# Optimization experiments

Hardware: AMD Instinct MI355X
Metric: run time of the kernel (lower is better)

Reference implementation:

```python
import jax, jax.numpy as jnp
import numpy as np

B = 2
D_MODEL = 256
D_FFN = 1024
N_LEVELS = 4
N_HEADS = 8
N_POINTS = 4
D_HEAD = D_MODEL // N_HEADS
SHAPES = np.array([[128, 128], [64, 64], [32, 32], [16, 16]], dtype=np.int32)  # (H, W) per level
LEN = int(SHAPES.prod(axis=1).sum())  # 21760
EPS = 1e-5


def _layer_norm(x, g, b):
    m = jnp.mean(x, axis=-1, keepdims=True)
    v = jnp.mean(jnp.square(x - m), axis=-1, keepdims=True)
    return (x - m) * jax.lax.rsqrt(v + EPS) * g + b


def _bilinear_gather(v_l, loc, H, W):
    # v_l: [B, H*W, NH, DH]; loc: [B, L, NH, NP, 2] in normalized [0,1] coords (x, y)
    # grid_sample(align_corners=False, padding_mode=zeros) semantics: pixel = loc * size - 0.5
    x = loc[..., 0] * W - 0.5
    y = loc[..., 1] * H - 0.5
    x0 = jnp.floor(x)
    y0 = jnp.floor(y)
    dx = x - x0
    dy = y - y0
    x0i = x0.astype(jnp.int32)
    y0i = y0.astype(jnp.int32)
    b_ix = jnp.arange(v_l.shape[0])[:, None, None, None]
    h_ix = jnp.arange(v_l.shape[2])[None, None, :, None]

    def corner(xi, yi, w):
        valid = (xi >= 0) & (xi < W) & (yi >= 0) & (yi < H)
        idx = jnp.clip(yi, 0, H - 1) * W + jnp.clip(xi, 0, W - 1)
        v = v_l[b_ix, idx, h_ix]  # [B, L, NH, NP, DH]
        return v * (w * valid.astype(v.dtype))[..., None]

    return (corner(x0i, y0i, (1 - dx) * (1 - dy))
            + corner(x0i + 1, y0i, dx * (1 - dy))
            + corner(x0i, y0i + 1, (1 - dx) * dy)
            + corner(x0i + 1, y0i + 1, dx * dy))


def _forward(src, pos, reference_points,
             w_off, b_off, w_attn, b_attn, w_val, b_val, w_out, b_out,
             ln1_g, ln1_b, w1, b1, w2, b2, ln2_g, ln2_b,
             spatial_shapes, level_start_index, padding_mask):
    shapes = np.asarray(spatial_shapes)        # static per-level (H, W)
    starts = np.asarray(level_start_index)     # static level offsets
    Bsz, L, _ = src.shape

    # ---- MSDeformAttn ----
    q = src + pos                              # with_pos_embed
    value = src @ w_val + b_val
    value = jnp.where(padding_mask[..., None], 0.0, value)
    value = value.reshape(Bsz, L, N_HEADS, D_HEAD)

    off = (q @ w_off + b_off).reshape(Bsz, L, N_HEADS, N_LEVELS, N_POINTS, 2)
    attn = (q @ w_attn + b_attn).reshape(Bsz, L, N_HEADS, N_LEVELS * N_POINTS)
    attn = jax.nn.softmax(attn, axis=-1).reshape(Bsz, L, N_HEADS, N_LEVELS, N_POINTS)

    wh = jnp.asarray(shapes[:, ::-1].copy(), dtype=src.dtype)  # [NL, 2] = (W, H)
    loc = reference_points[:, :, None, :, None, :] + off / wh[None, None, None, :, None, :]

    out = jnp.zeros((Bsz, L, N_HEADS, D_HEAD), src.dtype)
    for l in range(N_LEVELS):
        H, W = int(shapes[l, 0]), int(shapes[l, 1])
        s = int(starts[l])
        v_l = value[:, s:s + H * W]                          # [B, H*W, NH, DH]
        sampled = _bilinear_gather(v_l, loc[:, :, :, l], H, W)  # [B, L, NH, NP, DH]
        out = out + (sampled * attn[:, :, :, l][..., None]).sum(axis=3)
    attn_out = out.reshape(Bsz, L, D_MODEL) @ w_out + b_out

    # ---- residual + LN + FFN + residual + LN (dropout = identity in eval) ----
    x = _layer_norm(src + attn_out, ln1_g, ln1_b)
    ffn = jax.nn.relu(x @ w1 + b1) @ w2 + b2
    return _layer_norm(x + ffn, ln2_g, ln2_b)


def setup_inputs() -> dict:
    key = jax.random.key(0)
    ks = jax.random.split(key, 16)
    s = 0.02
    n_off = N_HEADS * N_LEVELS * N_POINTS
    level_start = np.concatenate([[0], SHAPES.prod(axis=1).cumsum()[:-1]]).astype(np.int32)
    return {
        "src": jax.random.normal(ks[0], (B, LEN, D_MODEL), jnp.float32),
        "pos": jax.random.normal(ks[1], (B, LEN, D_MODEL), jnp.float32),
        "reference_points": jax.random.uniform(ks[2], (B, LEN, N_LEVELS, 2), jnp.float32),
        "spatial_shapes": jnp.asarray(SHAPES),
        "level_start_index": jnp.asarray(level_start),
        "padding_mask": jnp.zeros((B, LEN), jnp.bool_),
        "w_off": jax.random.normal(ks[3], (D_MODEL, n_off * 2), jnp.float32) * s,
        "b_off": jax.random.normal(ks[4], (n_off * 2,), jnp.float32) * 0.5,
        "w_attn": jax.random.normal(ks[5], (D_MODEL, n_off), jnp.float32) * s,
        "b_attn": jnp.zeros((n_off,), jnp.float32),
        "w_val": jax.random.normal(ks[6], (D_MODEL, D_MODEL), jnp.float32) * s,
        "b_val": jnp.zeros((D_MODEL,), jnp.float32),
        "w_out": jax.random.normal(ks[7], (D_MODEL, D_MODEL), jnp.float32) * s,
        "b_out": jnp.zeros((D_MODEL,), jnp.float32),
        "ln1_g": jnp.ones((D_MODEL,), jnp.float32),
        "ln1_b": jnp.zeros((D_MODEL,), jnp.float32),
        "w1": jax.random.normal(ks[8], (D_MODEL, D_FFN), jnp.float32) * s,
        "b1": jnp.zeros((D_FFN,), jnp.float32),
        "w2": jax.random.normal(ks[9], (D_FFN, D_MODEL), jnp.float32) * s,
        "b2": jnp.zeros((D_MODEL,), jnp.float32),
        "ln2_g": jnp.ones((D_MODEL,), jnp.float32),
        "ln2_b": jnp.zeros((D_MODEL,), jnp.float32),
    }


def reference(src, pos, reference_points, spatial_shapes, level_start_index, padding_mask,
              w_off, b_off, w_attn, b_attn, w_val, b_val, w_out, b_out,
              ln1_g, ln1_b, w1, b1, w2, b2, ln2_g, ln2_b):
    return _forward(src, pos, reference_points,
                    w_off, b_off, w_attn, b_attn, w_val, b_val, w_out, b_out,
                    ln1_g, ln1_b, w1, b1, w2, b2, ln2_g, ln2_b,
                    spatial_shapes, level_start_index, padding_mask)
```

## Files before the change

kernel.cpp:

```cpp
#include <hip/hip_runtime.h>
#include <hip/hip_bf16.h>

#define BSZ      2
#define LTOK     21760
#define NTOK     (BSZ * LTOK)
#define DMODEL   256
#define DFFN     1024

typedef __attribute__((ext_vector_type(8))) short short8;
typedef __attribute__((ext_vector_type(4))) float f32x4;

__device__ __forceinline__ unsigned short f2bf(float x) {
    __hip_bfloat16 h = __float2bfloat16(x);
    return *reinterpret_cast<unsigned short*>(&h);
}
__device__ __forceinline__ float bf2f(unsigned short u) {
    union { unsigned int i; float f; } c; c.i = ((unsigned int)u) << 16; return c.f;
}
__device__ __forceinline__ float bflo(unsigned int u) {
    union { unsigned int i; float f; } c; c.i = u << 16; return c.f;
}
__device__ __forceinline__ float bfhi(unsigned int u) {
    union { unsigned int i; float f; } c; c.i = u & 0xffff0000u; return c.f;
}

#define TM 128
#define TN 256
#define TBK 32
#define EBS 264

__device__ __forceinline__ void gemm_core(
    const unsigned short* __restrict__ A,
    const unsigned short* __restrict__ Bt,
    unsigned short* sA, unsigned short* sB,
    int bm, int bn, int N, int K,
    int tid, int lane, int wm, int wn,
    f32x4 acc[4][8])
{
    const int sr = tid >> 6;
    const int fr = lane & 15;
    const int fk = (lane >> 4) * 8;

    for (int k0 = 0; k0 < K; k0 += TBK) {
        #pragma unroll
        for (int rr = 0; rr < 2; ++rr) {
            const int s = sr + rr * 4;
            const size_t grow = (size_t)(bm + s * 16 + fr);
            *(uint4*)&sA[s * 512 + lane * 8] = *(const uint4*)(A + grow * K + k0 + fk);
        }
        #pragma unroll
        for (int rr = 0; rr < 4; ++rr) {
            const int s = sr + rr * 4;
            int gn = bn + s * 16 + fr;
            gn = min(gn, N - 1);
            *(uint4*)&sB[s * 512 + lane * 8] = *(const uint4*)(Bt + (size_t)gn * K + k0 + fk);
        }
        __syncthreads();

        short8 af[4], bfr[8];
        #pragma unroll
        for (int i = 0; i < 4; ++i)
            af[i] = *(const short8*)&sA[(wm * 4 + i) * 512 + lane * 8];
        #pragma unroll
        for (int j = 0; j < 8; ++j)
            bfr[j] = *(const short8*)&sB[(wn * 8 + j) * 512 + lane * 8];
        #pragma unroll
        for (int i = 0; i < 4; ++i)
            #pragma unroll
            for (int j = 0; j < 8; ++j)
                acc[i][j] = __builtin_amdgcn_mfma_f32_16x16x32_bf16(
                    af[i], bfr[j], acc[i][j], 0, 0, 0);
        __syncthreads();
    }
}

__global__ __launch_bounds__(256, 2) void gemm_mfma(
    const unsigned short* __restrict__ A,
    const unsigned short* __restrict__ Bt, const float* __restrict__ bias,
    unsigned short* __restrict__ Cb,
    int M, int N, int K, int relu)
{
    __shared__ __align__(16) unsigned short smem[TM * TBK + TN * TBK];
    const int tid  = threadIdx.x;
    const int lane = tid & 63;
    const int wave = tid >> 6;
    const int wm = wave >> 1, wn = wave & 1;
    const int bm = blockIdx.y * TM;
    const int bn = blockIdx.x * TN;

    f32x4 acc[4][8];
    #pragma unroll
    for (int i = 0; i < 4; ++i)
        #pragma unroll
        for (int j = 0; j < 8; ++j)
            acc[i][j] = (f32x4){0.f, 0.f, 0.f, 0.f};

    gemm_core(A, Bt, smem, smem + TM * TBK, bm, bn, N, K, tid, lane, wm, wn, acc);

    const int r0 = (lane >> 4) * 4;
    const int c0 = lane & 15;
    unsigned short* eb = smem;
    #pragma unroll
    for (int i = 0; i < 4; ++i) {
        if (i) __syncthreads();
        #pragma unroll
        for (int j = 0; j < 8; ++j) {
            const int col = bn + wn * 128 + j * 16 + c0;
            const float bj = (col < N) ? bias[col] : 0.f;
            #pragma unroll
            for (int r = 0; r < 4; ++r) {
                float v = acc[i][j][r] + bj;
                if (relu) v = fmaxf(v, 0.f);
                eb[(wm * 16 + r0 + r) * EBS + wn * 128 + j * 16 + c0] = f2bf(v);
            }
        }
        __syncthreads();
        #pragma unroll
        for (int qq = 0; qq < 4; ++qq) {
            const int q  = tid + qq * 256;
            const int rl = q >> 5;
            const int ch = q & 31;
            const int grow = bm + (rl >> 4) * 64 + i * 16 + (rl & 15);
            const int colb = bn + ch * 8;
            if (colb < N)
                *(uint4*)&Cb[(size_t)grow * N + colb] =
                    *(const uint4*)&eb[rl * EBS + ch * 8];
        }
    }
}

__global__ __launch_bounds__(256, 2) void gemm_proj(
    const unsigned short* __restrict__ A0, const unsigned short* __restrict__ B0,
    const float* __restrict__ bias0, unsigned short* __restrict__ C0,
    const unsigned char* __restrict__ mask,
    const unsigned short* __restrict__ A1, const unsigned short* __restrict__ B1,
    const float* __restrict__ bias1, unsigned short* __restrict__ C1)
{
    __shared__ __align__(16) unsigned short smem[TM * TBK + TN * TBK];
    const int tid  = threadIdx.x;
    const int lane = tid & 63;
    const int wave = tid >> 6;
    const int wm = wave >> 1, wn = wave & 1;
    const int bm = blockIdx.y * TM;
    const int bx = blockIdx.x;

    const int isv = (bx == 0);
    const unsigned short* A    = isv ? A0 : A1;
    const unsigned short* Bt   = isv ? B0 : B1;
    const float*          bias = isv ? bias0 : bias1;
    const int N  = isv ? 256 : 384;
    const int bn = isv ? 0 : (bx - 1) * 256;
    const int K  = 256;

    f32x4 acc[4][8];
    #pragma unroll
    for (int i = 0; i < 4; ++i)
        #pragma unroll
        for (int j = 0; j < 8; ++j)
            acc[i][j] = (f32x4){0.f, 0.f, 0.f, 0.f};

    gemm_core(A, Bt, smem, smem + TM * TBK, bm, bn, N, K, tid, lane, wm, wn, acc);

    const int r0 = (lane >> 4) * 4;
    const int c0 = lane & 15;
    unsigned short* eb = smem;
    #pragma unroll
    for (int i = 0; i < 4; ++i) {
        if (i) __syncthreads();
        #pragma unroll
        for (int j = 0; j < 8; ++j) {
            const int col = bn + wn * 128 + j * 16 + c0;
            const float bj = (col < N) ? bias[col] : 0.f;
            #pragma unroll
            for (int r = 0; r < 4; ++r) {
                const int row = bm + wm * 64 + i * 16 + r0 + r;
                float v = acc[i][j][r] + bj;
                if (isv && mask[row]) v = 0.f;
                eb[(wm * 16 + r0 + r) * EBS + wn * 128 + j * 16 + c0] = f2bf(v);
            }
        }
        __syncthreads();
        #pragma unroll
        for (int qq = 0; qq < 4; ++qq) {
            const int q  = tid + qq * 256;
            const int rl = q >> 5;
            const int ch = q & 31;
            const int grow = bm + (rl >> 4) * 64 + i * 16 + (rl & 15);
            const int colb = bn + ch * 8;
            if (colb < N) {
                const uint4 val = *(const uint4*)&eb[rl * EBS + ch * 8];
                if (isv) {
                    const int bb   = grow >= LTOK;
                    const int srow = grow - bb * LTOK;
                    const int hcol = ch >> 2;
                    const int d    = (ch & 3) * 8;
                    *(uint4*)&C0[((size_t)(bb * 8 + hcol) * LTOK + srow) * 32 + d] = val;
                } else {
                    *(uint4*)&C1[(size_t)grow * 384 + colb] = val;
                }
            }
        }
    }
}

__global__ __launch_bounds__(256, 2) void gemm_ln(
    const unsigned short* __restrict__ A,
    const unsigned short* __restrict__ Bt, const float* __restrict__ bias,
    const unsigned short* __restrict__ resid,
    const float* __restrict__ g, const float* __restrict__ be,
    float* __restrict__ outF, unsigned short* __restrict__ outB, int K)
{
    __shared__ __align__(16) unsigned short smem[TM * TBK + TN * TBK];
    const int tid  = threadIdx.x;
    const int lane = tid & 63;
    const int wave = tid >> 6;
    const int wm = wave >> 1, wn = wave & 1;
    const int bm = blockIdx.y * TM;

    f32x4 acc[4][8];
    #pragma unroll
    for (int i = 0; i < 4; ++i)
        #pragma unroll
        for (int j = 0; j < 8; ++j)
            acc[i][j] = (f32x4){0.f, 0.f, 0.f, 0.f};

    gemm_core(A, Bt, smem, smem + TM * TBK, bm, 0, 256, K, tid, lane, wm, wn, acc);

    const int r0 = (lane >> 4) * 4;
    const int c0 = lane & 15;
    unsigned short* eb = smem;

    #pragma unroll
    for (int i = 0; i < 4; ++i) {
        if (i) __syncthreads();
        #pragma unroll
        for (int j = 0; j < 8; ++j) {
            const int col = wn * 128 + j * 16 + c0;
            const float bj = bias[col];
            #pragma unroll
            for (int r = 0; r < 4; ++r)
                eb[(wm * 16 + r0 + r) * EBS + col] = f2bf(acc[i][j][r] + bj);
        }
        __syncthreads();

        const int row = tid >> 3;
        const int l   = tid & 7;
        const int grow = bm + (row >> 4) * 64 + i * 16 + (row & 15);
        const unsigned short* rr = resid + (size_t)grow * 256 + l * 32;

        float s = 0.f, sq = 0.f;
        #pragma unroll
        for (int k = 0; k < 4; ++k) {
            const uint4 e = *(const uint4*)&eb[row * EBS + l * 32 + k * 8];
            const uint4 rv = *(const uint4*)(rr + k * 8);
            const unsigned int eu[4] = {e.x, e.y, e.z, e.w};
            const unsigned int ru[4] = {rv.x, rv.y, rv.z, rv.w};
            #pragma unroll
            for (int q = 0; q < 4; ++q) {
                const float v0 = bflo(eu[q]) + bflo(ru[q]);
                const float v1 = bfhi(eu[q]) + bfhi(ru[q]);
                s += v0 + v1;
                sq += v0 * v0 + v1 * v1;
            }
        }
        #pragma unroll
        for (int m = 4; m; m >>= 1) {
            s  += __shfl_xor(s, m, 8);
            sq += __shfl_xor(sq, m, 8);
        }
        const float mean = s * (1.f / 256.f);
        const float var  = sq * (1.f / 256.f) - mean * mean;
        const float rs   = rsqrtf(var + 1e-5f);

        #pragma unroll
        for (int k = 0; k < 4; ++k) {
            const int col = l * 32 + k * 8;
            const uint4 e = *(const uint4*)&eb[row * EBS + col];
            const uint4 rv = *(const uint4*)(rr + k * 8);
            const unsigned int eu[4] = {e.x, e.y, e.z, e.w};
            const unsigned int ru[4] = {rv.x, rv.y, rv.z, rv.w};
            float o[8];
            #pragma unroll
            for (int q = 0; q < 4; ++q) {
                const float g0 = g[col + q * 2],     b0 = be[col + q * 2];
                const float g1 = g[col + q * 2 + 1], b1 = be[col + q * 2 + 1];
                o[q * 2]     = (bflo(eu[q]) + bflo(ru[q]) - mean) * rs * g0 + b0;
                o[q * 2 + 1] = (bfhi(eu[q]) + bfhi(ru[q]) - mean) * rs * g1 + b1;
            }
            if (outB) {
                uint4 pk;
                pk.x = (unsigned)f2bf(o[0]) | ((unsigned)f2bf(o[1]) << 16);
                pk.y = (unsigned)f2bf(o[2]) | ((unsigned)f2bf(o[3]) << 16);
                pk.z = (unsigned)f2bf(o[4]) | ((unsigned)f2bf(o[5]) << 16);
                pk.w = (unsigned)f2bf(o[6]) | ((unsigned)f2bf(o[7]) << 16);
                *(uint4*)(outB + (size_t)grow * 256 + col) = pk;
            } else {
                float4 f0 = make_float4(o[0], o[1], o[2], o[3]);
                float4 f1 = make_float4(o[4], o[5], o[6], o[7]);
                *(float4*)(outF + (size_t)grow * 256 + col) = f0;
                *(float4*)(outF + (size_t)grow * 256 + col + 4) = f1;
            }
        }
        __syncthreads();
    }
}

__global__ __launch_bounds__(256) void prepass(
    const float* __restrict__ src, const float* __restrict__ pos,
    unsigned short* __restrict__ sb, unsigned short* __restrict__ qs)
{
    const size_t i = ((size_t)blockIdx.x * 256 + threadIdx.x) * 4;
    const float4 s = *(const float4*)(src + i);
    const float4 p = *(const float4*)(pos + i);
    ushort4 us, uq;
    us.x = f2bf(s.x); us.y = f2bf(s.y); us.z = f2bf(s.z); us.w = f2bf(s.w);
    uq.x = f2bf(s.x + p.x); uq.y = f2bf(s.y + p.y);
    uq.z = f2bf(s.z + p.z); uq.w = f2bf(s.w + p.w);
    *(ushort4*)(sb + i) = us;
    *(ushort4*)(qs + i) = uq;
}

__global__ void transpose_all(
    const float* __restrict__ w_val, const float* __restrict__ w_off,
    const float* __restrict__ w_att, const float* __restrict__ w_out,
    const float* __restrict__ w1,    const float* __restrict__ w2,
    const float* __restrict__ b_off, const float* __restrict__ b_att,
    unsigned short* __restrict__ wvalT, unsigned short* __restrict__ woaT,
    unsigned short* __restrict__ woutT, unsigned short* __restrict__ w1T,
    unsigned short* __restrict__ w2T,   float* __restrict__ bcat)
{
    const int blk = blockIdx.x;
    const int tx = threadIdx.x, ty = threadIdx.y;
    if (blk == 736) {
        const int t = ty * 32 + tx;
        bcat[t] = (t < 256) ? b_off[t] : b_att[t - 256];
        if (t + 256 < 384) bcat[t + 256] = b_att[t];
        return;
    }
    const float* W; unsigned short* Wt; int K, N, base;
    if      (blk < 64)  { W = w_val; Wt = wvalT;           K = 256;  N = 256;  base = 0;   }
    else if (blk < 128) { W = w_off; Wt = woaT;            K = 256;  N = 256;  base = 64;  }
    else if (blk < 160) { W = w_att; Wt = woaT + 256*256;  K = 256;  N = 128;  base = 128; }
    else if (blk < 224) { W = w_out; Wt = woutT;           K = 256;  N = 256;  base = 160; }
    else if (blk < 480) { W = w1;    Wt = w1T;             K = 256;  N = 1024; base = 224; }
    else                { W = w2;    Wt = w2T;             K = 1024; N = 256;  base = 480; }
    const int local = blk - base;
    const int kb = local % (K / 32);
    const int nb = local / (K / 32);
    const int k0 = kb * 32, n0 = nb * 32;

    __shared__ float t[32][33];
    #pragma unroll
    for (int i = 0; i < 32; i += 8)
        t[ty + i][tx] = W[(size_t)(k0 + ty + i) * N + n0 + tx];
    __syncthreads();
    #pragma unroll
    for (int i = 0; i < 32; i += 8)
        Wt[(size_t)(n0 + ty + i) * K + k0 + tx] = f2bf(t[tx][ty + i]);
}

__global__ __launch_bounds__(256) void sample_kernel(
    const unsigned short* __restrict__ vT, const unsigned short* __restrict__ qp,
    const float* __restrict__ ref,
    const int* __restrict__ sshapes, const int* __restrict__ lstart,
    unsigned short* __restrict__ samp)
{
    __shared__ __align__(16) int   s_o[256][4];
    __shared__ __align__(16) float s_w[256][4];

    const int blk   = blockIdx.x;
    const int plane = blk & 15;
    const int chunk = blk >> 4;
    const int b = plane >> 3;
    const int h = plane & 7;
    const int s0 = chunk * 16;
    const int t = threadIdx.x;

    {
        const int tl = t >> 4;
        const int p  = t & 15;
        const int l  = p >> 2;
        const int pp = p & 3;
        const int H = sshapes[2 * l], W = sshapes[2 * l + 1];
        const float Wf = (float)W, Hf = (float)H;
        const size_t tok = (size_t)(b * LTOK + s0 + tl);

        const float ox = bf2f(qp[tok * 384 + h * 32 + l * 8 + pp * 2 + 0]);
        const float oy = bf2f(qp[tok * 384 + h * 32 + l * 8 + pp * 2 + 1]);
        const float rx = ref[tok * 8 + l * 2 + 0];
        const float ry = ref[tok * 8 + l * 2 + 1];

        const float x = (rx + ox / Wf) * Wf - 0.5f;
        const float y = (ry + oy / Hf) * Hf - 0.5f;
        const float x0 = floorf(x), y0 = floorf(y);
        const float dx = x - x0, dy = y - y0;
        const int x0i = (int)x0, y0i = (int)y0;
        const int s = lstart[l];

        const float a = bf2f(qp[tok * 384 + 256 + h * 16 + p]);
        float mx = a;
        #pragma unroll
        for (int m = 8; m; m >>= 1) mx = fmaxf(mx, __shfl_xor(mx, m, 16));
        const float e = __expf(a - mx);
        float ssum = e;
        #pragma unroll
        for (int m = 8; m; m >>= 1) ssum += __shfl_xor(ssum, m, 16);
        const float prob = e / ssum;

        const float cw[4] = {(1.f - dx) * (1.f - dy), dx * (1.f - dy),
                             (1.f - dx) * dy,         dx * dy};
        const int cx[4] = {x0i, x0i + 1, x0i,     x0i + 1};
        const int cy[4] = {y0i, y0i,     y0i + 1, y0i + 1};
        int4   o4;
        float4 w4;
        #pragma unroll
        for (int c = 0; c < 4; ++c) {
            const bool valid = (cx[c] >= 0) & (cx[c] < W) & (cy[c] >= 0) & (cy[c] < H);
            const int xi = min(max(cx[c], 0), W - 1);
            const int yi = min(max(cy[c], 0), H - 1);
            ((int*)&o4)[c]   = (s + yi * W + xi) * 64;
            ((float*)&w4)[c] = valid ? cw[c] * prob : 0.f;
        }
        const int r = p * 16 + tl;
        *(int4*)&s_o[r][0]   = o4;
        *(float4*)&s_w[r][0] = w4;
    }
    __syncthreads();

    const int tl = t >> 4;
    const int dp = t & 15;
    const char* vp = (const char*)(vT + (size_t)plane * LTOK * 32) + dp * 4;
    float acc0 = 0.f, acc1 = 0.f;
    #pragma unroll
    for (int p = 0; p < 16; ++p) {
        const int r = p * 16 + tl;
        const int4   o4 = *(const int4*)&s_o[r][0];
        const float4 w4 = *(const float4*)&s_w[r][0];
        const unsigned int u0 = *(const unsigned int*)(vp + o4.x);
        const unsigned int u1 = *(const unsigned int*)(vp + o4.y);
        const unsigned int u2 = *(const unsigned int*)(vp + o4.z);
        const unsigned int u3 = *(const unsigned int*)(vp + o4.w);
        acc0 = fmaf(w4.x, bflo(u0), acc0); acc1 = fmaf(w4.x, bfhi(u0), acc1);
        acc0 = fmaf(w4.y, bflo(u1), acc0); acc1 = fmaf(w4.y, bfhi(u1), acc1);
        acc0 = fmaf(w4.z, bflo(u2), acc0); acc1 = fmaf(w4.z, bfhi(u2), acc1);
        acc0 = fmaf(w4.w, bflo(u3), acc0); acc1 = fmaf(w4.w, bfhi(u3), acc1);
    }
    const unsigned int o = (unsigned)f2bf(acc0) | ((unsigned)f2bf(acc1) << 16);
    *(unsigned int*)(samp + (size_t)(b * LTOK + s0 + tl) * 256 + h * 32 + dp * 2) = o;
}

extern "C" void kernel_launch(void* const* d_in, const int* in_sizes, int n_in,
                              void* d_out, int out_size, void* d_ws, size_t ws_size,
                              hipStream_t stream)
{
    const float* src   = (const float*)d_in[0];
    const float* pos   = (const float*)d_in[1];
    const float* ref   = (const float*)d_in[2];
    const int*   sshap = (const int*)d_in[3];
    const int*   lstrt = (const int*)d_in[4];
    const unsigned char* mask = (const unsigned char*)d_in[5];
    const float* w_off = (const float*)d_in[6];
    const float* b_off = (const float*)d_in[7];
    const float* w_att = (const float*)d_in[8];
    const float* b_att = (const float*)d_in[9];
    const float* w_val = (const float*)d_in[10];
    const float* b_val = (const float*)d_in[11];
    const float* w_out = (const float*)d_in[12];
    const float* b_out = (const float*)d_in[13];
    const float* ln1g  = (const float*)d_in[14];
    const float* ln1b  = (const float*)d_in[15];
    const float* w1    = (const float*)d_in[16];
    const float* b1    = (const float*)d_in[17];
    const float* w2    = (const float*)d_in[18];
    const float* b2    = (const float*)d_in[19];
    const float* ln2g  = (const float*)d_in[20];
    const float* ln2b  = (const float*)d_in[21];
    float* out = (float*)d_out;

    const size_t HSZ = (size_t)NTOK * 256 * 2;
    char* w = (char*)d_ws;
    unsigned short* qs     = (unsigned short*)w;
    unsigned short* samp16 = (unsigned short*)w;
    unsigned short* qpb    = (unsigned short*)(w + HSZ);
    unsigned short* vT     = (unsigned short*)(w + HSZ * 5 / 2);
    unsigned short* hidb   = (unsigned short*)w;
    unsigned short* sb     = (unsigned short*)(w + HSZ * 9 / 2);
    unsigned short* xb     = (unsigned short*)(w + HSZ * 11 / 2);
    char* wreg = w + HSZ * 13 / 2;
    unsigned short* wvalT  = (unsigned short*)wreg;
    unsigned short* woaT   = wvalT + 256 * 256;
    unsigned short* woutT  = woaT + 384 * 256;
    unsigned short* w1T    = woutT + 256 * 256;
    unsigned short* w2T    = w1T + 1024 * 256;
    float*          bcat   = (float*)(w2T + 256 * 1024);

    const dim3 blk(256);

    prepass<<<dim3(NTOK / 4), blk, 0, stream>>>(src, pos, sb, qs);

    transpose_all<<<dim3(737), dim3(32, 8), 0, stream>>>(
        w_val, w_off, w_att, w_out, w1, w2, b_off, b_att,
        wvalT, woaT, woutT, w1T, w2T, bcat);

    gemm_proj<<<dim3(3, NTOK / TM), blk, 0, stream>>>(
        sb, wvalT, b_val, vT, mask, qs, woaT, bcat, qpb);

    sample_kernel<<<dim3(16 * (LTOK / 16)), blk, 0, stream>>>(
        vT, qpb, ref, sshap, lstrt, samp16);

    gemm_ln<<<dim3(1, NTOK / TM), blk, 0, stream>>>(
        samp16, woutT, b_out, sb, ln1g, ln1b, nullptr, xb, 256);

    gemm_mfma<<<dim3(4, NTOK / TM), blk, 0, stream>>>(
        xb, w1T, b1, hidb, NTOK, DFFN, 256, 1);

    gemm_ln<<<dim3(1, NTOK / TM), blk, 0, stream>>>(
        hidb, w2T, b2, xb, ln2g, ln2b, out, nullptr, DFFN);
}
```

Before: 480.4 us.

## Double-buffer GEMM LDS tiles with direct global-to-LDS async loads

The shared GEMM core now loads tiles with global_load_lds, which writes straight into LDS without going through registers, and keeps two LDS buffers so the next K-tile is fetched while MFMAs run on the current one. Row pointers are computed once outside the K loop. The aim is to hide global memory latency and cut the register traffic in the GEMM kernels. In exchange LDS use per block doubles, which may lower occupancy, and correctness relies on the ordering of the async LDS writes and waits around the barriers.

```diff
diff --git a/kernel.cpp b/kernel.cpp
--- a/kernel.cpp
+++ b/kernel.cpp
@@ -24,15 +24,55 @@
     union { unsigned int i; float f; } c; c.i = u & 0xffff0000u; return c.f;
 }
 
+__device__ __forceinline__ void gload_lds16(const void* g, void* l) {
+    __builtin_amdgcn_global_load_lds(
+        (const __attribute__((address_space(1))) unsigned int*)g,
+        (__attribute__((address_space(3))) unsigned int*)l, 16, 0, 0);
+}
+
 #define TM 128
 #define TN 256
 #define TBK 32
+#define BUFSZ (TM * TBK + TN * TBK)
 #define EBS 264
+
+__device__ __forceinline__ void stage_tile(
+    const unsigned short* aR0, const unsigned short* aR1,
+    const unsigned short* bR0, const unsigned short* bR1,
+    const unsigned short* bR2, const unsigned short* bR3,
+    int k0, unsigned short* sA, unsigned short* sB, int sr)
+{
+    gload_lds16(aR0 + k0, &sA[(sr + 0)  * 512]);
+    gload_lds16(aR1 + k0, &sA[(sr + 4)  * 512]);
+    gload_lds16(bR0 + k0, &sB[(sr + 0)  * 512]);
+    gload_lds16(bR1 + k0, &sB[(sr + 4)  * 512]);
+    gload_lds16(bR2 + k0, &sB[(sr + 8)  * 512]);
+    gload_lds16(bR3 + k0, &sB[(sr + 12) * 512]);
+}
+
+__device__ __forceinline__ void compute_tile(
+    const unsigned short* sA, const unsigned short* sB,
+    int lane, int wm, int wn, f32x4 acc[4][8])
+{
+    short8 af[4], bfr[8];
+    #pragma unroll
+    for (int i = 0; i < 4; ++i)
+        af[i] = *(const short8*)&sA[(wm * 4 + i) * 512 + lane * 8];
+    #pragma unroll
+    for (int j = 0; j < 8; ++j)
+        bfr[j] = *(const short8*)&sB[(wn * 8 + j) * 512 + lane * 8];
+    #pragma unroll
+    for (int i = 0; i < 4; ++i)
+        #pragma unroll
+        for (int j = 0; j < 8; ++j)
+            acc[i][j] = __builtin_amdgcn_mfma_f32_16x16x32_bf16(
+                af[i], bfr[j], acc[i][j], 0, 0, 0);
+}
 
 __device__ __forceinline__ void gemm_core(
     const unsigned short* __restrict__ A,
     const unsigned short* __restrict__ Bt,
-    unsigned short* sA, unsigned short* sB,
+    unsigned short* smem,
     int bm, int bn, int N, int K,
     int tid, int lane, int wm, int wn,
     f32x4 acc[4][8])
@@ -41,35 +81,29 @@
     const int fr = lane & 15;
     const int fk = (lane >> 4) * 8;
 
-    for (int k0 = 0; k0 < K; k0 += TBK) {
-        #pragma unroll
-        for (int rr = 0; rr < 2; ++rr) {
-            const int s = sr + rr * 4;
-            const size_t grow = (size_t)(bm + s * 16 + fr);
-            *(uint4*)&sA[s * 512 + lane * 8] = *(const uint4*)(A + grow * K + k0 + fk);
-        }
-        #pragma unroll
-        for (int rr = 0; rr < 4; ++rr) {
-            const int s = sr + rr * 4;
-            int gn = bn + s * 16 + fr;
-            gn = min(gn, N - 1);
-            *(uint4*)&sB[s * 512 + lane * 8] = *(const uint4*)(Bt + (size_t)gn * K + k0 + fk);
-        }
+    const unsigned short* aR0 = A + (size_t)(bm + (sr + 0) * 16 + fr) * K + fk;
+    const unsigned short* aR1 = A + (size_t)(bm + (sr + 4) * 16 + fr) * K + fk;
+    const unsigned short* bR0 = Bt + (size_t)min(bn + (sr + 0)  * 16 + fr, N - 1) * K + fk;
+    const unsigned short* bR1 = Bt + (size_t)min(bn + (sr + 4)  * 16 + fr, N - 1) * K + fk;
+    const unsigned short* bR2 = Bt + (size_t)min(bn + (sr + 8)  * 16 + fr, N - 1) * K + fk;
+    const unsigned short* bR3 = Bt + (size_t)min(bn + (sr + 12) * 16 + fr, N - 1) * K + fk;
+
+    unsigned short* sA0 = smem;
+    unsigned short* sB0 = smem + TM * TBK;
+    unsigned short* sA1 = smem + BUFSZ;
+    unsigned short* sB1 = smem + BUFSZ + TM * TBK;
+
+    stage_tile(aR0, aR1, bR0, bR1, bR2, bR3, 0, sA0, sB0, sr);
+    __syncthreads();
+
+    for (int k0 = 0; k0 < K; k0 += 2 * TBK) {
+        if (k0 + TBK < K)
+            stage_tile(aR0, aR1, bR0, bR1, bR2, bR3, k0 + TBK, sA1, sB1, sr);
+        compute_tile(sA0, sB0, lane, wm, wn, acc);
         __syncthreads();
-
-        short8 af[4], bfr[8];
-        #pragma unroll
-        for (int i = 0; i < 4; ++i)
-            af[i] = *(const short8*)&sA[(wm * 4 + i) * 512 + lane * 8];
-        #pragma unroll
-        for (int j = 0; j < 8; ++j)
-            bfr[j] = *(const short8*)&sB[(wn * 8 + j) * 512 + lane * 8];
-        #pragma unroll
-        for (int i = 0; i < 4; ++i)
-            #pragma unroll
-            for (int j = 0; j < 8; ++j)
-                acc[i][j] = __builtin_amdgcn_mfma_f32_16x16x32_bf16(
-                    af[i], bfr[j], acc[i][j], 0, 0, 0);
+        if (k0 + 2 * TBK < K)
+            stage_tile(aR0, aR1, bR0, bR1, bR2, bR3, k0 + 2 * TBK, sA0, sB0, sr);
+        compute_tile(sA1, sB1, lane, wm, wn, acc);
         __syncthreads();
     }
 }
@@ -80,7 +114,7 @@
     unsigned short* __restrict__ Cb,
     int M, int N, int K, int relu)
 {
-    __shared__ __align__(16) unsigned short smem[TM * TBK + TN * TBK];
+    __shared__ __align__(16) unsigned short smem[2 * BUFSZ];
     const int tid  = threadIdx.x;
     const int lane = tid & 63;
     const int wave = tid >> 6;
@@ -95,7 +129,7 @@
         for (int j = 0; j < 8; ++j)
             acc[i][j] = (f32x4){0.f, 0.f, 0.f, 0.f};
 
-    gemm_core(A, Bt, smem, smem + TM * TBK, bm, bn, N, K, tid, lane, wm, wn, acc);
+    gemm_core(A, Bt, smem, bm, bn, N, K, tid, lane, wm, wn, acc);
 
     const int r0 = (lane >> 4) * 4;
     const int c0 = lane & 15;
@@ -136,7 +170,7 @@
     const unsigned short* __restrict__ A1, const unsigned short* __restrict__ B1,
     const float* __restrict__ bias1, unsigned short* __restrict__ C1)
 {
-    __shared__ __align__(16) unsigned short smem[TM * TBK + TN * TBK];
+    __shared__ __align__(16) unsigned short smem[2 * BUFSZ];
     const int tid  = threadIdx.x;
     const int lane = tid & 63;
     const int wave = tid >> 6;
@@ -159,7 +193,7 @@
         for (int j = 0; j < 8; ++j)
             acc[i][j] = (f32x4){0.f, 0.f, 0.f, 0.f};
 
-    gemm_core(A, Bt, smem, smem + TM * TBK, bm, bn, N, K, tid, lane, wm, wn, acc);
+    gemm_core(A, Bt, smem, bm, bn, N, K, tid, lane, wm, wn, acc);
 
     const int r0 = (lane >> 4) * 4;
     const int c0 = lane & 15;
@@ -210,7 +244,7 @@
     const float* __restrict__ g, const float* __restrict__ be,
     float* __restrict__ outF, unsigned short* __restrict__ outB, int K)
 {
-    __shared__ __align__(16) unsigned short smem[TM * TBK + TN * TBK];
+    __shared__ __align__(16) unsigned short smem[2 * BUFSZ];
     const int tid  = threadIdx.x;
     const int lane = tid & 63;
     const int wave = tid >> 6;
@@ -224,7 +258,7 @@
         for (int j = 0; j < 8; ++j)
             acc[i][j] = (f32x4){0.f, 0.f, 0.f, 0.f};
 
-    gemm_core(A, Bt, smem, smem + TM * TBK, bm, 0, 256, K, tid, lane, wm, wn, acc);
+    gemm_core(A, Bt, smem, bm, 0, 256, K, tid, lane, wm, wn, acc);
 
     const int r0 = (lane >> 4) * 4;
     const int c0 = lane & 15;
```

Result: no change. 482.6 us (+0.5%).

## Use 512-thread GEMM blocks with direct global-to-LDS loads

Applied to the files above, without the earlier changes.

Doubles the GEMM workgroup size to 8 waves, so each wave owns a 64x64 output sub-tile instead of 64x128. This halves accumulator registers and allows more concurrent waves. Tile loads now use global_load_lds to write straight into shared memory without passing through registers. The epilogue and LayerNorm reductions are remapped to the new thread count. Smaller per-wave tiles mean more LDS fragment reads per MFMA, and there is still no double buffering.

```diff
diff --git a/kernel.cpp b/kernel.cpp
--- a/kernel.cpp
+++ b/kernel.cpp
@@ -24,6 +24,12 @@
     union { unsigned int i; float f; } c; c.i = u & 0xffff0000u; return c.f;
 }
 
+__device__ __forceinline__ void gload_lds16(const void* g, void* l) {
+    __builtin_amdgcn_global_load_lds(
+        (const __attribute__((address_space(1))) unsigned int*)g,
+        (__attribute__((address_space(3))) unsigned int*)l, 16, 0, 0);
+}
+
 #define TM 128
 #define TN 256
 #define TBK 32
@@ -32,49 +38,46 @@
 __device__ __forceinline__ void gemm_core(
     const unsigned short* __restrict__ A,
     const unsigned short* __restrict__ Bt,
-    unsigned short* sA, unsigned short* sB,
+    unsigned short* smem,
     int bm, int bn, int N, int K,
     int tid, int lane, int wm, int wn,
-    f32x4 acc[4][8])
+    f32x4 acc[4][4])
 {
     const int sr = tid >> 6;
     const int fr = lane & 15;
     const int fk = (lane >> 4) * 8;
 
+    const unsigned short* aR  = A  + (size_t)(bm + sr * 16 + fr) * K + fk;
+    const unsigned short* bR0 = Bt + (size_t)min(bn + sr * 16 + fr,       N - 1) * K + fk;
+    const unsigned short* bR1 = Bt + (size_t)min(bn + (sr + 8) * 16 + fr, N - 1) * K + fk;
+
+    unsigned short* sA = smem;
+    unsigned short* sB = smem + TM * TBK;
+
     for (int k0 = 0; k0 < K; k0 += TBK) {
-        #pragma unroll
-        for (int rr = 0; rr < 2; ++rr) {
-            const int s = sr + rr * 4;
-            const size_t grow = (size_t)(bm + s * 16 + fr);
-            *(uint4*)&sA[s * 512 + lane * 8] = *(const uint4*)(A + grow * K + k0 + fk);
-        }
-        #pragma unroll
-        for (int rr = 0; rr < 4; ++rr) {
-            const int s = sr + rr * 4;
-            int gn = bn + s * 16 + fr;
-            gn = min(gn, N - 1);
-            *(uint4*)&sB[s * 512 + lane * 8] = *(const uint4*)(Bt + (size_t)gn * K + k0 + fk);
-        }
+        gload_lds16(aR  + k0, &sA[sr * 512]);
+        gload_lds16(bR0 + k0, &sB[sr * 512]);
+        gload_lds16(bR1 + k0, &sB[(sr + 8) * 512]);
         __syncthreads();
 
-        short8 af[4], bfr[8];
+        short8 af[4], bfr[4];
         #pragma unroll
         for (int i = 0; i < 4; ++i)
             af[i] = *(const short8*)&sA[(wm * 4 + i) * 512 + lane * 8];
         #pragma unroll
-        for (int j = 0; j < 8; ++j)
-            bfr[j] = *(const short8*)&sB[(wn * 8 + j) * 512 + lane * 8];
+        for (int j = 0; j < 4; ++j)
+            bfr[j] = *(const short8*)&sB[(wn * 4 + j) * 512 + lane * 8];
         #pragma unroll
         for (int i = 0; i < 4; ++i)
             #pragma unroll
-            for (int j = 0; j < 8; ++j)
+            for (int j = 0; j < 4; ++j)
                 acc[i][j] = __builtin_amdgcn_mfma_f32_16x16x32_bf16(
                     af[i], bfr[j], acc[i][j], 0, 0, 0);
         __syncthreads();
     }
 }
 
-__global__ __launch_bounds__(256, 2) void gemm_mfma(
+__global__ __launch_bounds__(512, 4) void gemm_mfma(
     const unsigned short* __restrict__ A,
     const unsigned short* __restrict__ Bt, const float* __restrict__ bias,
     unsigned short* __restrict__ Cb,
@@ -84,18 +87,18 @@
     const int tid  = threadIdx.x;
     const int lane = tid & 63;
     const int wave = tid >> 6;
-    const int wm = wave >> 1, wn = wave & 1;
+    const int wm = wave >> 2, wn = wave & 3;
     const int bm = blockIdx.y * TM;
     const int bn = blockIdx.x * TN;
 
-    f32x4 acc[4][8];
+    f32x4 acc[4][4];
     #pragma unroll
     for (int i = 0; i < 4; ++i)
         #pragma unroll
-        for (int j = 0; j < 8; ++j)
+        for (int j = 0; j < 4; ++j)
             acc[i][j] = (f32x4){0.f, 0.f, 0.f, 0.f};
 
-    gemm_core(A, Bt, smem, smem + TM * TBK, bm, bn, N, K, tid, lane, wm, wn, acc);
+    gemm_core(A, Bt, smem, bm, bn, N, K, tid, lane, wm, wn, acc);
 
     const int r0 = (lane >> 4) * 4;
     const int c0 = lane & 15;
@@ -104,20 +107,20 @@
     for (int i = 0; i < 4; ++i) {
         if (i) __syncthreads();
         #pragma unroll
-        for (int j = 0; j < 8; ++j) {
-            const int col = bn + wn * 128 + j * 16 + c0;
+        for (int j = 0; j < 4; ++j) {
+            const int col = bn + wn * 64 + j * 16 + c0;
             const float bj = (col < N) ? bias[col] : 0.f;
             #pragma unroll
             for (int r = 0; r < 4; ++r) {
                 float v = acc[i][j][r] + bj;
                 if (relu) v = fmaxf(v, 0.f);
-                eb[(wm * 16 + r0 + r) * EBS + wn * 128 + j * 16 + c0] = f2bf(v);
+                eb[(wm * 16 + r0 + r) * EBS + wn * 64 + j * 16 + c0] = f2bf(v);
             }
         }
         __syncthreads();
         #pragma unroll
-        for (int qq = 0; qq < 4; ++qq) {
-            const int q  = tid + qq * 256;
+        for (int qq = 0; qq < 2; ++qq) {
+            const int q  = tid + qq * 512;
             const int rl = q >> 5;
             const int ch = q & 31;
             const int grow = bm + (rl >> 4) * 64 + i * 16 + (rl & 15);
@@ -129,7 +132,7 @@
     }
 }
 
-__global__ __launch_bounds__(256, 2) void gemm_proj(
+__global__ __launch_bounds__(512, 4) void gemm_proj(
     const unsigned short* __restrict__ A0, const unsigned short* __restrict__ B0,
     const float* __restrict__ bias0, unsigned short* __restrict__ C0,
     const unsigned char* __restrict__ mask,
@@ -140,7 +143,7 @@
     const int tid  = threadIdx.x;
     const int lane = tid & 63;
     const int wave = tid >> 6;
-    const int wm = wave >> 1, wn = wave & 1;
+    const int wm = wave >> 2, wn = wave & 3;
     const int bm = blockIdx.y * TM;
     const int bx = blockIdx.x;
 
@@ -152,14 +155,14 @@
     const int bn = isv ? 0 : (bx - 1) * 256;
     const int K  = 256;
 
-    f32x4 acc[4][8];
+    f32x4 acc[4][4];
     #pragma unroll
     for (int i = 0; i < 4; ++i)
         #pragma unroll
-        for (int j = 0; j < 8; ++j)
+        for (int j = 0; j < 4; ++j)
             acc[i][j] = (f32x4){0.f, 0.f, 0.f, 0.f};
 
-    gemm_core(A, Bt, smem, smem + TM * TBK, bm, bn, N, K, tid, lane, wm, wn, acc);
+    gemm_core(A, Bt, smem, bm, bn, N, K, tid, lane, wm, wn, acc);
 
     const int r0 = (lane >> 4) * 4;
     const int c0 = lane & 15;
@@ -168,21 +171,21 @@
     for (int i = 0; i < 4; ++i) {
         if (i) __syncthreads();
         #pragma unroll
-        for (int j = 0; j < 8; ++j) {
-            const int col = bn + wn * 128 + j * 16 + c0;
+        for (int j = 0; j < 4; ++j) {
+            const int col = bn + wn * 64 + j * 16 + c0;
             const float bj = (col < N) ? bias[col] : 0.f;
             #pragma unroll
             for (int r = 0; r < 4; ++r) {
                 const int row = bm + wm * 64 + i * 16 + r0 + r;
                 float v = acc[i][j][r] + bj;
                 if (isv && mask[row]) v = 0.f;
-                eb[(wm * 16 + r0 + r) * EBS + wn * 128 + j * 16 + c0] = f2bf(v);
+                eb[(wm * 16 + r0 + r) * EBS + wn * 64 + j * 16 + c0] = f2bf(v);
             }
         }
         __syncthreads();
         #pragma unroll
-        for (int qq = 0; qq < 4; ++qq) {
-            const int q  = tid + qq * 256;
+        for (int qq = 0; qq < 2; ++qq) {
+            const int q  = tid + qq * 512;
             const int rl = q >> 5;
             const int ch = q & 31;
             const int grow = bm + (rl >> 4) * 64 + i * 16 + (rl & 15);
@@ -203,7 +206,7 @@
     }
 }
 
-__global__ __launch_bounds__(256, 2) void gemm_ln(
+__global__ __launch_bounds__(512, 4) void gemm_ln(
     const unsigned short* __restrict__ A,
     const unsigned short* __restrict__ Bt, const float* __restrict__ bias,
     const unsigned short* __restrict__ resid,
@@ -214,17 +217,17 @@
     const int tid  = threadIdx.x;
     const int lane = tid & 63;
     const int wave = tid >> 6;
-    const int wm = wave >> 1, wn = wave & 1;
+    const int wm = wave >> 2, wn = wave & 3;
     const int bm = blockIdx.y * TM;
 
-    f32x4 acc[4][8];
+    f32x4 acc[4][4];
     #pragma unroll
     for (int i = 0; i < 4; ++i)
         #pragma unroll
-        for (int j = 0; j < 8; ++j)
+        for (int j = 0; j < 4; ++j)
             acc[i][j] = (f32x4){0.f, 0.f, 0.f, 0.f};
 
-    gemm_core(A, Bt, smem, smem + TM * TBK, bm, 0, 256, K, tid, lane, wm, wn, acc);
+    gemm_core(A, Bt, smem, bm, 0, 256, K, tid, lane, wm, wn, acc);
 
     const int r0 = (lane >> 4) * 4;
     const int c0 = lane & 15;
@@ -234,8 +237,8 @@
     for (int i = 0; i < 4; ++i) {
         if (i) __syncthreads();
         #pragma unroll
-        for (int j = 0; j < 8; ++j) {
-            const int col = wn * 128 + j * 16 + c0;
+        for (int j = 0; j < 4; ++j) {
+            const int col = wn * 64 + j * 16 + c0;
             const float bj = bias[col];
             #pragma unroll
             for (int r = 0; r < 4; ++r)
@@ -243,15 +246,15 @@
         }
         __syncthreads();
 
-        const int row = tid >> 3;
-        const int l   = tid & 7;
+        const int row = tid >> 4;
+        const int l   = tid & 15;
         const int grow = bm + (row >> 4) * 64 + i * 16 + (row & 15);
-        const unsigned short* rr = resid + (size_t)grow * 256 + l * 32;
+        const unsigned short* rr = resid + (size_t)grow * 256 + l * 16;
 
         float s = 0.f, sq = 0.f;
         #pragma unroll
-        for (int k = 0; k < 4; ++k) {
-            const uint4 e = *(const uint4*)&eb[row * EBS + l * 32 + k * 8];
+        for (int k = 0; k < 2; ++k) {
+            const uint4 e = *(const uint4*)&eb[row * EBS + l * 16 + k * 8];
             const uint4 rv = *(const uint4*)(rr + k * 8);
             const unsigned int eu[4] = {e.x, e.y, e.z, e.w};
             const unsigned int ru[4] = {rv.x, rv.y, rv.z, rv.w};
@@ -264,17 +267,17 @@
             }
         }
         #pragma unroll
-        for (int m = 4; m; m >>= 1) {
-            s  += __shfl_xor(s, m, 8);
-            sq += __shfl_xor(sq, m, 8);
+        for (int m = 8; m; m >>= 1) {
+            s  += __shfl_xor(s, m, 16);
+            sq += __shfl_xor(sq, m, 16);
         }
         const float mean = s * (1.f / 256.f);
         const float var  = sq * (1.f / 256.f) - mean * mean;
         const float rs   = rsqrtf(var + 1e-5f);
 
         #pragma unroll
-        for (int k = 0; k < 4; ++k) {
-            const int col = l * 32 + k * 8;
+        for (int k = 0; k < 2; ++k) {
+            const int col = l * 16 + k * 8;
             const uint4 e = *(const uint4*)&eb[row * EBS + col];
             const uint4 rv = *(const uint4*)(rr + k * 8);
             const unsigned int eu[4] = {e.x, e.y, e.z, e.w};
@@ -495,6 +498,7 @@
     float*          bcat   = (float*)(w2T + 256 * 1024);
 
     const dim3 blk(256);
+    const dim3 blk512(512);
 
     prepass<<<dim3(NTOK / 4), blk, 0, stream>>>(src, pos, sb, qs);
 
@@ -502,18 +506,18 @@
         w_val, w_off, w_att, w_out, w1, w2, b_off, b_att,
         wvalT, woaT, woutT, w1T, w2T, bcat);
 
-    gemm_proj<<<dim3(3, NTOK / TM), blk, 0, stream>>>(
+    gemm_proj<<<dim3(3, NTOK / TM), blk512, 0, stream>>>(
         sb, wvalT, b_val, vT, mask, qs, woaT, bcat, qpb);
 
     sample_kernel<<<dim3(16 * (LTOK / 16)), blk, 0, stream>>>(
         vT, qpb, ref, sshap, lstrt, samp16);
 
-    gemm_ln<<<dim3(1, NTOK / TM), blk, 0, stream>>>(
+    gemm_ln<<<dim3(1, NTOK / TM), blk512, 0, stream>>>(
         samp16, woutT, b_out, sb, ln1g, ln1b, nullptr, xb, 256);
 
-    gemm_mfma<<<dim3(4, NTOK / TM), blk, 0, stream>>>(
+    gemm_mfma<<<dim3(4, NTOK / TM), blk512, 0, stream>>>(
         xb, w1T, b1, hidb, NTOK, DFFN, 256, 1);
 
-    gemm_ln<<<dim3(1, NTOK / TM), blk, 0, stream>>>(
+    gemm_ln<<<dim3(1, NTOK / TM), blk512, 0, stream>>>(
         hidb, w2T, b2, xb, ln2g, ln2b, out, nullptr, DFFN);
 }
```

Result: faster. 463.5 us (-3.5%).

## Halve GEMM M-tile and load tiles via direct global-to-LDS transfers

Applied to the files above, without the earlier changes.

Shrinks the GEMM row tile from 128 to 64, cutting per-thread accumulators in half and raising launch bounds to allow four blocks per CU. Global loads of A and B tiles now go straight into LDS through the global_load_lds builtin instead of staging in registers, and row pointers are precomputed outside the K loop. The aim is higher occupancy and less register pressure to hide memory latency. In exchange each block reuses B less and the grid has twice as many blocks, and the direct-to-LDS layout must match the lane-contiguous pattern the MFMA fragment reads expect.

```diff
diff --git a/kernel.cpp b/kernel.cpp
--- a/kernel.cpp
+++ b/kernel.cpp
@@ -24,7 +24,13 @@
     union { unsigned int i; float f; } c; c.i = u & 0xffff0000u; return c.f;
 }
 
-#define TM 128
+__device__ __forceinline__ void gload_lds16(const void* g, void* l) {
+    __builtin_amdgcn_global_load_lds(
+        (const __attribute__((address_space(1))) unsigned int*)g,
+        (__attribute__((address_space(3))) unsigned int*)l, 16, 0, 0);
+}
+
+#define TM 64
 #define TN 256
 #define TBK 32
 #define EBS 264
@@ -32,49 +38,45 @@
 __device__ __forceinline__ void gemm_core(
     const unsigned short* __restrict__ A,
     const unsigned short* __restrict__ Bt,
-    unsigned short* sA, unsigned short* sB,
+    unsigned short* smem,
     int bm, int bn, int N, int K,
     int tid, int lane, int wm, int wn,
-    f32x4 acc[4][8])
+    f32x4 acc[2][8])
 {
     const int sr = tid >> 6;
     const int fr = lane & 15;
     const int fk = (lane >> 4) * 8;
 
+    const unsigned short* aR  = A  + (size_t)(bm + sr * 16 + fr) * K + fk;
+    const unsigned short* bR0 = Bt + (size_t)min(bn + (sr + 0)  * 16 + fr, N - 1) * K + fk;
+    const unsigned short* bR1 = Bt + (size_t)min(bn + (sr + 4)  * 16 + fr, N - 1) * K + fk;
+    const unsigned short* bR2 = Bt + (size_t)min(bn + (sr + 8)  * 16 + fr, N - 1) * K + fk;
+    const unsigned short* bR3 = Bt + (size_t)min(bn + (sr + 12) * 16 + fr, N - 1) * K + fk;
+
+    unsigned short* sA = smem;
+    unsigned short* sB = smem + TM * TBK;
+
     for (int k0 = 0; k0 < K; k0 += TBK) {
-        #pragma unroll
-        for (int rr = 0; rr < 2; ++rr) {
-            const int s = sr + rr * 4;
-            const size_t grow = (size_t)(bm + s * 16 + fr);
-            *(uint4*)&sA[s * 512 + lane * 8] = *(const uint4*)(A + grow * K + k0 + fk);
-        }
-        #pragma unroll
-        for (int rr = 0; rr < 4; ++rr) {
-            const int s = sr + rr * 4;
-            int gn = bn + s * 16 + fr;
-            gn = min(gn, N - 1);
-            *(uint4*)&sB[s * 512 + lane * 8] = *(const uint4*)(Bt + (size_t)gn * K + k0 + fk);
-        }
+        gload_lds16(aR  + k0, &sA[sr * 512]);
+        gload_lds16(bR0 + k0, &sB[(sr + 0)  * 512]);
+        gload_lds16(bR1 + k0, &sB[(sr + 4)  * 512]);
+        gload_lds16(bR2 + k0, &sB[(sr + 8)  * 512]);
+        gload_lds16(bR3 + k0, &sB[(sr + 12) * 512]);
         __syncthreads();
 
-        short8 af[4], bfr[8];
-        #pragma unroll
-        for (int i = 0; i < 4; ++i)
-            af[i] = *(const short8*)&sA[(wm * 4 + i) * 512 + lane * 8];
-        #pragma unroll
-        for (int j = 0; j < 8; ++j)
-            bfr[j] = *(const short8*)&sB[(wn * 8 + j) * 512 + lane * 8];
-        #pragma unroll
-        for (int i = 0; i < 4; ++i)
-            #pragma unroll
-            for (int j = 0; j < 8; ++j)
-                acc[i][j] = __builtin_amdgcn_mfma_f32_16x16x32_bf16(
-                    af[i], bfr[j], acc[i][j], 0, 0, 0);
+        short8 af0 = *(const short8*)&sA[(wm * 2 + 0) * 512 + lane * 8];
+        short8 af1 = *(const short8*)&sA[(wm * 2 + 1) * 512 + lane * 8];
+        #pragma unroll
+        for (int j = 0; j < 8; ++j) {
+            const short8 bfr = *(const short8*)&sB[(wn * 8 + j) * 512 + lane * 8];
+            acc[0][j] = __builtin_amdgcn_mfma_f32_16x16x32_bf16(af0, bfr, acc[0][j], 0, 0, 0);
+            acc[1][j] = __builtin_amdgcn_mfma_f32_16x16x32_bf16(af1, bfr, acc[1][j], 0, 0, 0);
+        }
         __syncthreads();
     }
 }
 
-__global__ __launch_bounds__(256, 2) void gemm_mfma(
+__global__ __launch_bounds__(256, 4) void gemm_mfma(
     const unsigned short* __restrict__ A,
     const unsigned short* __restrict__ Bt, const float* __restrict__ bias,
     unsigned short* __restrict__ Cb,
@@ -88,20 +90,20 @@
     const int bm = blockIdx.y * TM;
     const int bn = blockIdx.x * TN;
 
-    f32x4 acc[4][8];
-    #pragma unroll
-    for (int i = 0; i < 4; ++i)
+    f32x4 acc[2][8];
+    #pragma unroll
+    for (int i = 0; i < 2; ++i)
         #pragma unroll
         for (int j = 0; j < 8; ++j)
             acc[i][j] = (f32x4){0.f, 0.f, 0.f, 0.f};
 
-    gemm_core(A, Bt, smem, smem + TM * TBK, bm, bn, N, K, tid, lane, wm, wn, acc);
+    gemm_core(A, Bt, smem, bm, bn, N, K, tid, lane, wm, wn, acc);
 
     const int r0 = (lane >> 4) * 4;
     const int c0 = lane & 15;
     unsigned short* eb = smem;
     #pragma unroll
-    for (int i = 0; i < 4; ++i) {
+    for (int i = 0; i < 2; ++i) {
         if (i) __syncthreads();
         #pragma unroll
         for (int j = 0; j < 8; ++j) {
@@ -120,7 +122,7 @@
             const int q  = tid + qq * 256;
             const int rl = q >> 5;
             const int ch = q & 31;
-            const int grow = bm + (rl >> 4) * 64 + i * 16 + (rl & 15);
+            const int grow = bm + (rl >> 4) * 32 + i * 16 + (rl & 15);
             const int colb = bn + ch * 8;
             if (colb < N)
                 *(uint4*)&Cb[(size_t)grow * N + colb] =
@@ -129,7 +131,7 @@
     }
 }
 
-__global__ __launch_bounds__(256, 2) void gemm_proj(
+__global__ __launch_bounds__(256, 4) void gemm_proj(
     const unsigned short* __restrict__ A0, const unsigned short* __restrict__ B0,
     const float* __restrict__ bias0, unsigned short* __restrict__ C0,
     const unsigned char* __restrict__ mask,
@@ -152,20 +154,20 @@
     const int bn = isv ? 0 : (bx - 1) * 256;
     const int K  = 256;
 
-    f32x4 acc[4][8];
-    #pragma unroll
-    for (int i = 0; i < 4; ++i)
+    f32x4 acc[2][8];
+    #pragma unroll
+    for (int i = 0; i < 2; ++i)
         #pragma unroll
         for (int j = 0; j < 8; ++j)
             acc[i][j] = (f32x4){0.f, 0.f, 0.f, 0.f};
 
-    gemm_core(A, Bt, smem, smem + TM * TBK, bm, bn, N, K, tid, lane, wm, wn, acc);
+    gemm_core(A, Bt, smem, bm, bn, N, K, tid, lane, wm, wn, acc);
 
     const int r0 = (lane >> 4) * 4;
     const int c0 = lane & 15;
     unsigned short* eb = smem;
     #pragma unroll
-    for (int i = 0; i < 4; ++i) {
+    for (int i = 0; i < 2; ++i) {
         if (i) __syncthreads();
         #pragma unroll
         for (int j = 0; j < 8; ++j) {
@@ -173,7 +175,7 @@
             const float bj = (col < N) ? bias[col] : 0.f;
             #pragma unroll
             for (int r = 0; r < 4; ++r) {
-                const int row = bm + wm * 64 + i * 16 + r0 + r;
+                const int row = bm + wm * 32 + i * 16 + r0 + r;
                 float v = acc[i][j][r] + bj;
                 if (isv && mask[row]) v = 0.f;
                 eb[(wm * 16 + r0 + r) * EBS + wn * 128 + j * 16 + c0] = f2bf(v);
@@ -185,7 +187,7 @@
             const int q  = tid + qq * 256;
             const int rl = q >> 5;
             const int ch = q & 31;
-            const int grow = bm + (rl >> 4) * 64 + i * 16 + (rl & 15);
+            const int grow = bm + (rl >> 4) * 32 + i * 16 + (rl & 15);
             const int colb = bn + ch * 8;
             if (colb < N) {
                 const uint4 val = *(const uint4*)&eb[rl * EBS + ch * 8];
@@ -203,7 +205,7 @@
     }
 }
 
-__global__ __launch_bounds__(256, 2) void gemm_ln(
+__global__ __launch_bounds__(256, 4) void gemm_ln(
     const unsigned short* __restrict__ A,
     const unsigned short* __restrict__ Bt, const float* __restrict__ bias,
     const unsigned short* __restrict__ resid,
@@ -217,21 +219,21 @@
     const int wm = wave >> 1, wn = wave & 1;
     const int bm = blockIdx.y * TM;
 
-    f32x4 acc[4][8];
-    #pragma unroll
-    for (int i = 0; i < 4; ++i)
+    f32x4 acc[2][8];
+    #pragma unroll
+    for (int i = 0; i < 2; ++i)
         #pragma unroll
         for (int j = 0; j < 8; ++j)
             acc[i][j] = (f32x4){0.f, 0.f, 0.f, 0.f};
 
-    gemm_core(A, Bt, smem, smem + TM * TBK, bm, 0, 256, K, tid, lane, wm, wn, acc);
+    gemm_core(A, Bt, smem, bm, 0, 256, K, tid, lane, wm, wn, acc);
 
     const int r0 = (lane >> 4) * 4;
     const int c0 = lane & 15;
     unsigned short* eb = smem;
 
     #pragma unroll
-    for (int i = 0; i < 4; ++i) {
+    for (int i = 0; i < 2; ++i) {
         if (i) __syncthreads();
         #pragma unroll
         for (int j = 0; j < 8; ++j) {
@@ -245,7 +247,7 @@
 
         const int row = tid >> 3;
         const int l   = tid & 7;
-        const int grow = bm + (row >> 4) * 64 + i * 16 + (row & 15);
+        const int grow = bm + (row >> 4) * 32 + i * 16 + (row & 15);
         const unsigned short* rr = resid + (size_t)grow * 256 + l * 32;
 
         float s = 0.f, sq = 0.f;
```

After: 497.6 us. 1.04x slower.
